# Kernel optimization log

Hardware: AMD Instinct MI355X
Metric: run time of the kernel (lower is better)

Reference implementation:

```python
import jax, jax.numpy as jnp
import numpy as np

PAD_IDX = 1          # OpenNMT PAD_WORD index in tgt_dict
BATCH = 32
TLEN = 64
SLEN = 400
CVOCAB = 100
D = 512
VOCAB = 32000
NEG_INF = -1e9       # stand-in for -inf so softmax stays grad-safe


def setup_inputs() -> dict:
    key = jax.random.key(0)
    k1, k2, k3, k4, k5 = jax.random.split(key, 5)
    hidden = jax.random.normal(k1, (BATCH * TLEN, D), dtype=jnp.float32)
    # attention distribution over source positions
    attn = jax.nn.softmax(jax.random.normal(k2, (BATCH * TLEN, SLEN), dtype=jnp.float32), axis=-1)
    # src_map: one-hot indicator routing each source position to an extended-vocab slot
    idx = jax.random.randint(k3, (SLEN, BATCH), 0, CVOCAB)
    src_map = jax.nn.one_hot(idx, CVOCAB, dtype=jnp.float32)  # [slen, batch, cvocab]
    W = jax.random.normal(k4, (D, VOCAB), dtype=jnp.float32) * 0.02
    b = jnp.zeros((VOCAB,), dtype=jnp.float32)
    Wc = jax.random.normal(k5, (D, 1), dtype=jnp.float32) * 0.02
    bc = jnp.zeros((1,), dtype=jnp.float32)
    return {"hidden": hidden, "attn": attn, "src_map": src_map,
            "W": W, "b": b, "Wc": Wc, "bc": bc}


def reference(hidden, attn, src_map, W, b, Wc, bc):
    # standard generator softmax over tgt vocab, PAD masked out
    logits = hidden @ W + b                                   # [B*T, V]
    logits = logits.at[:, PAD_IDX].set(NEG_INF)
    prob = jax.nn.softmax(logits, axis=1)
    # copy switch p(z)
    p_copy = jax.nn.sigmoid(hidden @ Wc + bc)                 # [B*T, 1]
    out_prob = prob * (1.0 - p_copy)                          # [B*T, V]
    mul_attn = attn * p_copy                                  # [B*T, slen]
    # route attention mass into extended vocab via src_map (tlen-major layout)
    mul_attn_t = mul_attn.reshape(TLEN, BATCH, SLEN)          # [tlen, batch, slen]
    copy_prob = jnp.einsum('tbs,sbc->tbc', mul_attn_t, src_map)  # [tlen, batch, cvocab]
    copy_prob = copy_prob.reshape(-1, CVOCAB)                 # [B*T, cvocab]
    return jnp.concatenate([out_prob, copy_prob], axis=1)
```

## Files before the change

kernel.cpp:

```cpp
#include <hip/hip_runtime.h>

#define PAD_IDX 1
#define BATCH 32
#define TLEN 64
#define SLEN 400
#define CVOCAB 100
#define DDIM 512
#define VOCAB 32000
#define ROWS (BATCH * TLEN)
#define OUTC (VOCAB + CVOCAB)

typedef float f32x4 __attribute__((ext_vector_type(4)));
typedef __bf16 bf16x8 __attribute__((ext_vector_type(8)));

__device__ __forceinline__ unsigned short f32_to_bf16_rne(float f) {
    union { float f; unsigned u; } x; x.f = f;
    return (unsigned short)((x.u + 0x7FFFu + ((x.u >> 16) & 1u)) >> 16);
}

__global__ void k_convert_hidden(const float* __restrict__ hid,
                                 unsigned short* __restrict__ a_bf) {
    int i = blockIdx.x * 256 + threadIdx.x;
    const float4 v = reinterpret_cast<const float4*>(hid)[i];
    ushort4 o;
    o.x = f32_to_bf16_rne(v.x); o.y = f32_to_bf16_rne(v.y);
    o.z = f32_to_bf16_rne(v.z); o.w = f32_to_bf16_rne(v.w);
    reinterpret_cast<ushort4*>(a_bf)[i] = o;
}

__global__ void k_transpose_w(const float* __restrict__ W,
                              unsigned short* __restrict__ Wt) {
    __shared__ float tile[32][33];
    const int nx = threadIdx.x;
    const int ky = threadIdx.y;
    const int n0 = blockIdx.x * 32;
    const int k0 = blockIdx.y * 32;
#pragma unroll
    for (int j = 0; j < 4; ++j)
        tile[ky + 8 * j][nx] = W[(k0 + ky + 8 * j) * VOCAB + n0 + nx];
    __syncthreads();
#pragma unroll
    for (int j = 0; j < 4; ++j) {
        int n = ky + 8 * j;
        Wt[(n0 + n) * DDIM + k0 + nx] = f32_to_bf16_rne(tile[nx][n]);
    }
}

__global__ void k_pcopy(const float* __restrict__ hid, const float* __restrict__ Wc,
                        const float* __restrict__ bc, float* __restrict__ p_copy,
                        float* __restrict__ row_sum) {
    const int tid = threadIdx.x;
    const int lane = tid & 63;
    const int wv = tid >> 6;
    const int r = blockIdx.x * 4 + wv;
    float s = 0.f;
#pragma unroll
    for (int j = 0; j < 8; ++j)
        s += hid[r * DDIM + lane + 64 * j] * Wc[lane + 64 * j];
#pragma unroll
    for (int off = 32; off >= 1; off >>= 1)
        s += __shfl_xor(s, off);
    if (lane == 0) {
        float z = s + bc[0];
        p_copy[r] = 1.f / (1.f + __expf(-z));
        row_sum[r] = 0.f;
    }
}

__global__ void k_gemm_exp(const unsigned short* __restrict__ A,
                           const unsigned short* __restrict__ Bt,
                           const float* __restrict__ bias,
                           float* __restrict__ out,
                           float* __restrict__ row_sum) {
    __shared__ __align__(16) unsigned short ldsA[128 * 64];
    __shared__ __align__(16) unsigned short ldsB[128 * 64];

    const int tid = threadIdx.x;
    const int lane = tid & 63;
    const int wv = tid >> 6;
    const int wm = wv >> 1, wn = wv & 1;
    const int m0 = blockIdx.y * 128;
    const int n0 = blockIdx.x * 128;
    const int g = lane >> 4;
    const int c16 = lane & 15;

    f32x4 acc[4][4];
#pragma unroll
    for (int mi = 0; mi < 4; ++mi)
#pragma unroll
        for (int ni = 0; ni < 4; ++ni)
            acc[mi][ni] = (f32x4){0.f, 0.f, 0.f, 0.f};

    for (int ks = 0; ks < 8; ++ks) {
        const int k0 = ks * 64;
#pragma unroll
        for (int it = 0; it < 4; ++it) {
            const int ci = it * 256 + wv * 64 + lane;
            const int row = ci >> 3;
            const int seg = (ci & 7) ^ (row & 7);
            const unsigned short* gA = A + (m0 + row) * DDIM + k0 + seg * 8;
            const unsigned short* gB = Bt + (n0 + row) * DDIM + k0 + seg * 8;
            __builtin_amdgcn_global_load_lds(
                (const __attribute__((address_space(1))) void*)gA,
                (__attribute__((address_space(3))) void*)(ldsA + (it * 256 + wv * 64) * 8),
                16, 0, 0);
            __builtin_amdgcn_global_load_lds(
                (const __attribute__((address_space(1))) void*)gB,
                (__attribute__((address_space(3))) void*)(ldsB + (it * 256 + wv * 64) * 8),
                16, 0, 0);
        }
        __syncthreads();
#pragma unroll
        for (int kk = 0; kk < 2; ++kk) {
            bf16x8 af[4], bf[4];
#pragma unroll
            for (int mi = 0; mi < 4; ++mi) {
                const int row = wm * 64 + mi * 16 + c16;
                const int s16 = (kk * 4 + g) ^ (row & 7);
                af[mi] = *reinterpret_cast<const bf16x8*>(ldsA + row * 64 + s16 * 8);
            }
#pragma unroll
            for (int ni = 0; ni < 4; ++ni) {
                const int row = wn * 64 + ni * 16 + c16;
                const int s16 = (kk * 4 + g) ^ (row & 7);
                bf[ni] = *reinterpret_cast<const bf16x8*>(ldsB + row * 64 + s16 * 8);
            }
#pragma unroll
            for (int mi = 0; mi < 4; ++mi)
#pragma unroll
                for (int ni = 0; ni < 4; ++ni)
                    acc[mi][ni] = __builtin_amdgcn_mfma_f32_16x16x32_bf16(
                        af[mi], bf[ni], acc[mi][ni], 0, 0, 0);
        }
        __syncthreads();
    }

    float bias_v[4];
    int gcol[4];
#pragma unroll
    for (int ni = 0; ni < 4; ++ni) {
        gcol[ni] = n0 + wn * 64 + ni * 16 + c16;
        bias_v[ni] = bias[gcol[ni]];
    }
    float part[4][4];
#pragma unroll
    for (int mi = 0; mi < 4; ++mi)
#pragma unroll
        for (int v = 0; v < 4; ++v)
            part[mi][v] = 0.f;

#pragma unroll
    for (int mi = 0; mi < 4; ++mi) {
#pragma unroll
        for (int ni = 0; ni < 4; ++ni) {
#pragma unroll
            for (int v = 0; v < 4; ++v) {
                const int grow = m0 + wm * 64 + mi * 16 + g * 4 + v;
                float val = acc[mi][ni][v] + bias_v[ni];
                val = (gcol[ni] == PAD_IDX) ? 0.f : __expf(val);
                out[grow * OUTC + gcol[ni]] = val;
                part[mi][v] += val;
            }
        }
    }
#pragma unroll
    for (int mi = 0; mi < 4; ++mi) {
#pragma unroll
        for (int v = 0; v < 4; ++v) {
            float p = part[mi][v];
            p += __shfl_xor(p, 1);
            p += __shfl_xor(p, 2);
            p += __shfl_xor(p, 4);
            p += __shfl_xor(p, 8);
            if (c16 == 0)
                atomicAdd(&row_sum[m0 + wm * 64 + mi * 16 + g * 4 + v], p);
        }
    }
}

__global__ void k_scale(float* __restrict__ out, const float* __restrict__ p_copy,
                        const float* __restrict__ row_sum) {
    const int r = blockIdx.y;
    const int c4 = blockIdx.x * 256 + threadIdx.x;
    if (c4 >= VOCAB / 4) return;
    const float s = (1.f - p_copy[r]) / row_sum[r];
    float4* p = reinterpret_cast<float4*>(out + (size_t)r * OUTC) + c4;
    float4 v = *p;
    v.x *= s; v.y *= s; v.z *= s; v.w *= s;
    *p = v;
}

__global__ void k_copy(const float* __restrict__ attn, const float* __restrict__ src_map,
                       const float* __restrict__ p_copy, float* __restrict__ out) {
    const int tid = threadIdx.x;
    const int lane = tid & 63;
    const int wv = tid >> 6;
    const int r = blockIdx.x * 4 + wv;
    const int b = r & (BATCH - 1);
    float acc0 = 0.f, acc1 = 0.f;
    const float* srcb = src_map + b * CVOCAB;
    const float* arow = attn + r * SLEN;
    for (int s0 = 0; s0 < SLEN; s0 += 64) {
        const float av = (s0 + lane < SLEN) ? arow[s0 + lane] : 0.f;
        const int lim = min(64, SLEN - s0);
        for (int i = 0; i < lim; ++i) {
            const float a = __shfl(av, i);
            const float* sp = srcb + (size_t)(s0 + i) * (BATCH * CVOCAB);
            acc0 += a * sp[lane];
            if (lane < CVOCAB - 64) acc1 += a * sp[lane + 64];
        }
    }
    const float pc = p_copy[r];
    float* orow = out + (size_t)r * OUTC + VOCAB;
    orow[lane] = pc * acc0;
    if (lane + 64 < CVOCAB) orow[lane + 64] = pc * acc1;
}

extern "C" void kernel_launch(void* const* d_in, const int* in_sizes, int n_in,
                              void* d_out, int out_size, void* d_ws, size_t ws_size,
                              hipStream_t stream) {
    const float* hidden = (const float*)d_in[0];
    const float* attn   = (const float*)d_in[1];
    const float* srcmap = (const float*)d_in[2];
    const float* W      = (const float*)d_in[3];
    const float* bias   = (const float*)d_in[4];
    const float* Wc     = (const float*)d_in[5];
    const float* bc     = (const float*)d_in[6];
    float* out = (float*)d_out;

    char* ws = (char*)d_ws;
    size_t off = 0;
    unsigned short* a_bf = (unsigned short*)(ws + off); off += (size_t)ROWS * DDIM * 2;
    unsigned short* wt   = (unsigned short*)(ws + off); off += (size_t)VOCAB * DDIM * 2;
    float* p_copy = (float*)(ws + off); off += (size_t)ROWS * 4;
    float* row_sum = (float*)(ws + off); off += (size_t)ROWS * 4;
    if (ws_size < off) return;

    k_convert_hidden<<<(ROWS * DDIM / 4 + 255) / 256, 256, 0, stream>>>(hidden, a_bf);
    k_transpose_w<<<dim3(VOCAB / 32, DDIM / 32), dim3(32, 8), 0, stream>>>(W, wt);
    k_pcopy<<<ROWS / 4, 256, 0, stream>>>(hidden, Wc, bc, p_copy, row_sum);
    k_gemm_exp<<<dim3(VOCAB / 128, ROWS / 128), 256, 0, stream>>>(a_bf, wt, bias, out, row_sum);
    k_scale<<<dim3((VOCAB / 4 + 255) / 256, ROWS), 256, 0, stream>>>(out, p_copy, row_sum);
    k_copy<<<ROWS / 4, 256, 0, stream>>>(attn, srcmap, p_copy, out);
}
```

Before: 808.3 us.

## Store bf16 logits in-place and fuse softmax normalization into per-row kernel

The GEMM now writes bias-added logits as bf16 into the first half of each output row instead of fp32 exp values, and it drops the atomic row-sum reduction. A new per-row kernel loads the bf16 row into LDS, computes the exp sum, then writes normalized fp32 probabilities back over the same row. This replaces the separate scale pass and halves the GEMM's output traffic. The GEMM grid is also remapped to a 1D swizzled order to improve L2 reuse of weight tiles. The copy loop gets an unroll pragma. Rounding logits to bf16 before exp adds precision error, and the softmax still does not subtract the row max, so large logits could overflow.

```diff
diff --git a/kernel.cpp b/kernel.cpp
--- a/kernel.cpp
+++ b/kernel.cpp
@@ -17,6 +17,10 @@
     union { float f; unsigned u; } x; x.f = f;
     return (unsigned short)((x.u + 0x7FFFu + ((x.u >> 16) & 1u)) >> 16);
 }
+__device__ __forceinline__ float bf16_to_f32(unsigned short h) {
+    union { unsigned u; float f; } x; x.u = ((unsigned)h) << 16;
+    return x.f;
+}
 
 __global__ void k_convert_hidden(const float* __restrict__ hid,
                                  unsigned short* __restrict__ a_bf) {
@@ -47,8 +51,7 @@
 }
 
 __global__ void k_pcopy(const float* __restrict__ hid, const float* __restrict__ Wc,
-                        const float* __restrict__ bc, float* __restrict__ p_copy,
-                        float* __restrict__ row_sum) {
+                        const float* __restrict__ bc, float* __restrict__ p_copy) {
     const int tid = threadIdx.x;
     const int lane = tid & 63;
     const int wv = tid >> 6;
@@ -63,15 +66,13 @@
     if (lane == 0) {
         float z = s + bc[0];
         p_copy[r] = 1.f / (1.f + __expf(-z));
-        row_sum[r] = 0.f;
-    }
-}
-
-__global__ void k_gemm_exp(const unsigned short* __restrict__ A,
-                           const unsigned short* __restrict__ Bt,
-                           const float* __restrict__ bias,
-                           float* __restrict__ out,
-                           float* __restrict__ row_sum) {
+    }
+}
+
+__global__ void k_gemm(const unsigned short* __restrict__ A,
+                       const unsigned short* __restrict__ Bt,
+                       const float* __restrict__ bias,
+                       float* __restrict__ out) {
     __shared__ __align__(16) unsigned short ldsA[128 * 64];
     __shared__ __align__(16) unsigned short ldsB[128 * 64];
 
@@ -79,8 +80,12 @@
     const int lane = tid & 63;
     const int wv = tid >> 6;
     const int wm = wv >> 1, wn = wv & 1;
-    const int m0 = blockIdx.y * 128;
-    const int n0 = blockIdx.x * 128;
+
+    const int bid = blockIdx.x;
+    const int lin = (bid & 7) * 500 + (bid >> 3);
+    const int m0 = (lin & 15) * 128;
+    const int n0 = (lin >> 4) * 128;
+
     const int g = lane >> 4;
     const int c16 = lane & 15;
 
@@ -135,6 +140,7 @@
         __syncthreads();
     }
 
+    unsigned short* outu = reinterpret_cast<unsigned short*>(out);
     float bias_v[4];
     int gcol[4];
 #pragma unroll
@@ -142,52 +148,81 @@
         gcol[ni] = n0 + wn * 64 + ni * 16 + c16;
         bias_v[ni] = bias[gcol[ni]];
     }
-    float part[4][4];
-#pragma unroll
-    for (int mi = 0; mi < 4; ++mi)
-#pragma unroll
-        for (int v = 0; v < 4; ++v)
-            part[mi][v] = 0.f;
-
 #pragma unroll
     for (int mi = 0; mi < 4; ++mi) {
 #pragma unroll
-        for (int ni = 0; ni < 4; ++ni) {
-#pragma unroll
-            for (int v = 0; v < 4; ++v) {
-                const int grow = m0 + wm * 64 + mi * 16 + g * 4 + v;
-                float val = acc[mi][ni][v] + bias_v[ni];
-                val = (gcol[ni] == PAD_IDX) ? 0.f : __expf(val);
-                out[grow * OUTC + gcol[ni]] = val;
-                part[mi][v] += val;
-            }
-        }
-    }
-#pragma unroll
-    for (int mi = 0; mi < 4; ++mi) {
-#pragma unroll
         for (int v = 0; v < 4; ++v) {
-            float p = part[mi][v];
-            p += __shfl_xor(p, 1);
-            p += __shfl_xor(p, 2);
-            p += __shfl_xor(p, 4);
-            p += __shfl_xor(p, 8);
-            if (c16 == 0)
-                atomicAdd(&row_sum[m0 + wm * 64 + mi * 16 + g * 4 + v], p);
-        }
-    }
-}
-
-__global__ void k_scale(float* __restrict__ out, const float* __restrict__ p_copy,
-                        const float* __restrict__ row_sum) {
-    const int r = blockIdx.y;
-    const int c4 = blockIdx.x * 256 + threadIdx.x;
-    if (c4 >= VOCAB / 4) return;
-    const float s = (1.f - p_copy[r]) / row_sum[r];
-    float4* p = reinterpret_cast<float4*>(out + (size_t)r * OUTC) + c4;
-    float4 v = *p;
-    v.x *= s; v.y *= s; v.z *= s; v.w *= s;
-    *p = v;
+            const size_t rbase = (size_t)(m0 + wm * 64 + mi * 16 + g * 4 + v) * (OUTC * 2);
+#pragma unroll
+            for (int ni = 0; ni < 4; ++ni)
+                outu[rbase + gcol[ni]] = f32_to_bf16_rne(acc[mi][ni][v] + bias_v[ni]);
+        }
+    }
+}
+
+__global__ void __launch_bounds__(512) k_rowsoft(float* __restrict__ out,
+                                                 const float* __restrict__ p_copy) {
+    __shared__ __align__(16) unsigned short srow[VOCAB];
+    __shared__ float red[8];
+    const int tid = threadIdx.x;
+    const int r = blockIdx.x;
+    const uint4* lrow = reinterpret_cast<const uint4*>(out + (size_t)r * OUTC);
+    uint4* srow16 = reinterpret_cast<uint4*>(srow);
+
+#pragma unroll
+    for (int it = 0; it < 4; ++it) {
+        const int idx = it * 512 + tid;
+        if (idx < 2000) {
+            srow16[idx * 2]     = lrow[idx * 2];
+            srow16[idx * 2 + 1] = lrow[idx * 2 + 1];
+        }
+    }
+    __syncthreads();
+
+    float ps = 0.f;
+#pragma unroll
+    for (int it = 0; it < 4; ++it) {
+        const int idx = it * 512 + tid;
+        if (idx < 2000) {
+            const int c0 = idx * 16;
+#pragma unroll
+            for (int j = 0; j < 16; ++j) {
+                const int c = c0 + j;
+                const float l = bf16_to_f32(srow[c]);
+                ps += (c == PAD_IDX) ? 0.f : __expf(l);
+            }
+        }
+    }
+#pragma unroll
+    for (int off = 32; off >= 1; off >>= 1)
+        ps += __shfl_xor(ps, off);
+    if ((tid & 63) == 0) red[tid >> 6] = ps;
+    __syncthreads();
+    float sum = 0.f;
+#pragma unroll
+    for (int w = 0; w < 8; ++w) sum += red[w];
+
+    const float scale = (1.f - p_copy[r]) / sum;
+    float* orow = out + (size_t)r * OUTC;
+#pragma unroll
+    for (int it = 0; it < 4; ++it) {
+        const int idx = it * 512 + tid;
+        if (idx < 2000) {
+            const int c0 = idx * 16;
+#pragma unroll
+            for (int q = 0; q < 4; ++q) {
+                float4 o;
+                float* po = &o.x;
+#pragma unroll
+                for (int j = 0; j < 4; ++j) {
+                    const int c = c0 + q * 4 + j;
+                    const float l = bf16_to_f32(srow[c]);
+                    po[j] = (c == PAD_IDX) ? 0.f : __expf(l) * scale;
+                }
+                reinterpret_cast<float4*>(orow + c0)[q] = o;
+            }
+        }
+    }
 }
 
 __global__ void k_copy(const float* __restrict__ attn, const float* __restrict__ src_map,
@@ -203,6 +238,7 @@
     for (int s0 = 0; s0 < SLEN; s0 += 64) {
         const float av = (s0 + lane < SLEN) ? arow[s0 + lane] : 0.f;
         const int lim = min(64, SLEN - s0);
+#pragma unroll 8
         for (int i = 0; i < lim; ++i) {
             const float a = __shfl(av, i);
             const float* sp = srcb + (size_t)(s0 + i) * (BATCH * CVOCAB);
@@ -233,13 +269,12 @@
     unsigned short* a_bf = (unsigned short*)(ws + off); off += (size_t)ROWS * DDIM * 2;
     unsigned short* wt   = (unsigned short*)(ws + off); off += (size_t)VOCAB * DDIM * 2;
     float* p_copy = (float*)(ws + off); off += (size_t)ROWS * 4;
-    float* row_sum = (float*)(ws + off); off += (size_t)ROWS * 4;
     if (ws_size < off) return;
 
     k_convert_hidden<<<(ROWS * DDIM / 4 + 255) / 256, 256, 0, stream>>>(hidden, a_bf);
     k_transpose_w<<<dim3(VOCAB / 32, DDIM / 32), dim3(32, 8), 0, stream>>>(W, wt);
-    k_pcopy<<<ROWS / 4, 256, 0, stream>>>(hidden, Wc, bc, p_copy, row_sum);
-    k_gemm_exp<<<dim3(VOCAB / 128, ROWS / 128), 256, 0, stream>>>(a_bf, wt, bias, out, row_sum);
-    k_scale<<<dim3((VOCAB / 4 + 255) / 256, ROWS), 256, 0, stream>>>(out, p_copy, row_sum);
+    k_pcopy<<<ROWS / 4, 256, 0, stream>>>(hidden, Wc, bc, p_copy);
+    k_gemm<<<4000, 256, 0, stream>>>(a_bf, wt, bias, out);
+    k_rowsoft<<<ROWS, 512, 0, stream>>>(out, p_copy);
     k_copy<<<ROWS / 4, 256, 0, stream>>>(attn, srcmap, p_copy, out);
 }
```

New measurement: 661.0 us. 18.2% less time.
